# Kernel tuning notes

Measured on AMD Instinct MI355X. Metric: run time of the kernel, lower is better.

Reference implementation:

```python
import jax, jax.numpy as jnp
import numpy as np

B, T, N = 16, 1024, 128
WIN, STEP = 30, 2
MOMENT_ORDERS = (2, 4, 8)
D_MODEL = 256


def _mask_diag(corr):
    n = corr.shape[-1]
    eye = jnp.eye(n, dtype=corr.dtype)
    return corr * (1.0 - eye) + eye


def corrcoef_time(xw):
    # xw: [..., L, N] -> corr over channels: [..., N, N]
    L = xw.shape[-2]
    xm = xw - xw.mean(axis=-2, keepdims=True)
    cov = jnp.einsum('...ln,...lm->...nm', xm, xm) / (L - 1 + 1e-8)
    var = jnp.clip(jnp.diagonal(cov, axis1=-2, axis2=-1), 1e-8, None)
    std = jnp.sqrt(var)
    corr = cov / (std[..., :, None] * std[..., None, :])
    corr = jnp.nan_to_num(corr, nan=0.0, posinf=0.0, neginf=0.0)
    return _mask_diag(corr)


def rowwise_corr(M):
    # M: [B, N, F]
    Xc = M - M.mean(axis=-1, keepdims=True)
    num = jnp.einsum('bnf,bmf->bnm', Xc, Xc)
    den1 = jnp.sqrt(jnp.clip((Xc ** 2).sum(axis=-1), 1e-8, None))
    corr = num / (den1[:, :, None] * den1[:, None, :])
    corr = jnp.nan_to_num(corr, nan=0.0, posinf=0.0, neginf=0.0)
    return _mask_diag(corr)


def layer_norm(x, gamma, beta, eps=1e-5):
    mu = x.mean(axis=-1, keepdims=True)
    var = ((x - mu) ** 2).mean(axis=-1, keepdims=True)
    return (x - mu) / jnp.sqrt(var + eps) * gamma + beta


def normalize_adj(adj):
    n = adj.shape[-1]
    A_hat = adj + jnp.eye(n, dtype=adj.dtype)
    d = A_hat.sum(axis=-1)
    dis = jnp.sqrt(1.0 / jnp.clip(d, 1e-8, None))
    return A_hat * dis[:, :, None] * dis[:, None, :]


def setup_inputs() -> dict:
    key = jax.random.key(0)
    ks = jax.random.split(key, 8)
    in_dim = len(MOMENT_ORDERS) * N
    return {
        'x': jax.random.normal(ks[0], (B, T, N), dtype=jnp.float32),
        'ln_gamma': jnp.ones((in_dim,), jnp.float32),
        'ln_beta': jnp.zeros((in_dim,), jnp.float32),
        'W1': jax.random.normal(ks[1], (in_dim, D_MODEL), jnp.float32) * 0.05,
        'b1': jnp.zeros((D_MODEL,), jnp.float32),
        'W2': jax.random.normal(ks[2], (D_MODEL, D_MODEL), jnp.float32) * 0.05,
        'b2': jnp.zeros((D_MODEL,), jnp.float32),
        'Wc': jax.random.normal(ks[3], (D_MODEL, 1), jnp.float32) * 0.05,
        'bc': jnp.zeros((1,), jnp.float32),
    }


def reference(x, ln_gamma, ln_beta, W1, b1, W2, b2, Wc, bc):
    # sliding windows (static indices)
    starts = np.arange(0, T - WIN + 1, STEP)
    idx = starts[:, None] + np.arange(WIN)[None, :]
    xw = x[:, idx, :]
    lo = corrcoef_time(xw)                            # [B, Wn, N, N]

    mean_lo = lo.mean(axis=1, keepdims=True)
    centered = lo - mean_lo
    cm_list, ho_list = [], []
    for d in MOMENT_ORDERS:
        cm = jnp.nan_to_num((centered ** d).mean(axis=1),
                            nan=0.0, posinf=0.0, neginf=0.0)  # [B, N, N]
        cm_list.append(cm)
        ho_list.append(rowwise_corr(cm))

    X = jnp.concatenate(cm_list, axis=-1)             # [B, N, 3N]
    X = layer_norm(X, ln_gamma, ln_beta)

    A = jnp.stack(ho_list, axis=1).mean(axis=1)
    A = 0.5 * (A + jnp.swapaxes(A, 1, 2))
    A_norm = normalize_adj(A)

    H = jax.nn.relu(jnp.einsum('bnm,bmd->bnd', A_norm, X @ W1 + b1))
    H = jax.nn.relu(jnp.einsum('bnm,bmd->bnd', A_norm, H @ W2 + b2))
    g = H.mean(axis=1)                                # [B, d_model]
    out = jax.nn.sigmoid(g @ Wc + bc)                 # [B, 1]
    return out
```

## Files before the change

kernel.cpp:

```cpp
#include <hip/hip_runtime.h>
#include <math.h>

#define BB  16
#define TT  1024
#define NN  128
#define WIN 30
#define NWD 498
#define DM  256
#define IND 384
#define GW  16

#define INV_W (1.0f/498.0f)

#define SARR (BB*NN*NN)

#define OFF_A     0
#define OFF_G     (OFF_A    + BB*NWD*NN)
#define OFF_CM2   (OFF_G    + BB*NWD*NN)
#define OFF_CM4   (OFF_CM2  + SARR)
#define OFF_CM8   (OFF_CM4  + SARR)
#define OFF_AD    (OFF_CM8  + SARR)
#define OFF_PART  (OFF_AD   + 3*SARR)
#define OFF_ANORM OFF_PART
#define OFF_BUFA  (OFF_ANORM + SARR)
#define OFF_BUFB  (OFF_BUFA + BB*NN*DM)
#define OFF_CTR   (OFF_PART + 768*16384)

#define GLL16(gsrc, ldst) \
    __builtin_amdgcn_global_load_lds((const __attribute__((address_space(1))) void*)(gsrc), \
                                     (__attribute__((address_space(3))) void*)(ldst), 16, 0, 0)

__global__ __launch_bounds__(128) void k1_stats(const float* __restrict__ x, float* __restrict__ ws) {
    int bx = blockIdx.x;
    if (bx == 0 && threadIdx.x < 128) ((unsigned*)(ws + OFF_CTR))[threadIdx.x] = 0u;
    int c = bx & 15, b = bx >> 4;
    int w0 = c*32, w1 = min(NWD, w0+32);
    int n = threadIdx.x;
    const float* xp = x + (size_t)b*TT*NN + n;

    float sum = 0.f, sq = 0.f;
    for (int t = 2*w0; t < 2*w0 + WIN; ++t) {
        float v = xp[(size_t)t*NN];
        sum += v; sq = fmaf(v, v, sq);
    }
    for (int w = w0; w < w1; ++w) {
        if (w > w0) {
            float o0 = xp[(size_t)(2*w-2)*NN], o1 = xp[(size_t)(2*w-1)*NN];
            float n0 = xp[(size_t)(2*w+28)*NN], n1 = xp[(size_t)(2*w+29)*NN];
            sum += (n0 + n1) - (o0 + o1);
            sq  += (n0*n0 + n1*n1) - (o0*o0 + o1*o1);
        }
        float mean = sum * (1.0f/30.0f);
        float ss = sq - 30.0f*mean*mean;
        float var = fmaxf(ss * (1.0f/29.0f), 1e-8f);
        float a = (1.0f / sqrtf(var)) * 0.185695338f;
        ws[OFF_A + ((size_t)b*NWD + w)*NN + n] = a;
        ws[OFF_G + ((size_t)b*NWD + w)*NN + n] = mean * a * 5.477225575f;
    }
}

__global__ __launch_bounds__(256) __attribute__((amdgpu_waves_per_eu(3, 3)))
void k24_inc(const float* __restrict__ x, float* __restrict__ ws) {
    __shared__ __align__(16) float xr[64][NN];
    __shared__ __align__(16) float sa[GW][NN];
    __shared__ __align__(16) float sg[GW][NN];
    int bx = blockIdx.x;
    int wc = bx & 7;
    int slab = (bx >> 3) % 6;
    int b = bx / 48;
    const char IS[6] = {0,0,0,0,1,1};
    const char JS[6] = {0,1,2,3,2,3};
    int is = IS[slab], js = JS[slab];
    int w0 = wc * 63, w1 = min(NWD, w0 + 63);
    int tid = threadIdx.x;
    int jg = tid & 7, ig = tid >> 3;
    int i0 = is*64 + ig*2;
    int j0 = js*32 + jg*4;

    const float* xb = x + (size_t)b*TT*NN;
    const float* Ab = ws + OFF_A + (size_t)b*NWD*NN;
    const float* Gb = ws + OFF_G + (size_t)b*NWD*NN;

    float P[2][4];
    float S1[2][4], S2[2][4], S3[2][4], S4[2][4], S5[2][4], S6[2][4], S7[2][4], S8[2][4];
#pragma unroll
    for (int p=0;p<2;++p)
#pragma unroll
        for (int q=0;q<4;++q) {
            P[p][q]=0.f;
            S1[p][q]=0.f;S2[p][q]=0.f;S3[p][q]=0.f;S4[p][q]=0.f;
            S5[p][q]=0.f;S6[p][q]=0.f;S7[p][q]=0.f;S8[p][q]=0.f;
        }

    auto moments = [&](int k) {
        float2 ai = *(const float2*)&sa[k][i0];
        float2 gi = *(const float2*)&sg[k][i0];
        float4 aj = *(const float4*)&sa[k][j0];
        float4 gj = *(const float4*)&sg[k][j0];
        float av[2] = {ai.x, ai.y};
        float mg[2] = {-gi.x, -gi.y};
        float aw[4] = {aj.x, aj.y, aj.z, aj.w};
        float gw[4] = {gj.x, gj.y, gj.z, gj.w};
#pragma unroll
        for (int p=0;p<2;++p)
#pragma unroll
            for (int q=0;q<4;++q) {
                float aa  = av[p]*aw[q];
                float ngg = mg[p]*gw[q];
                float c   = fmaf(P[p][q], aa, ngg);
                float c2 = c*c;
                float c3 = c2*c;
                float c4 = c2*c2;
                S1[p][q] += c;
                S2[p][q] += c2;
                S3[p][q] += c3;
                S4[p][q] += c4;
                S5[p][q] = fmaf(c4, c,  S5[p][q]);
                S6[p][q] = fmaf(c3, c3, S6[p][q]);
                S7[p][q] = fmaf(c3, c4, S7[p][q]);
                S8[p][q] = fmaf(c4, c4, S8[p][q]);
            }
    };

    int rlo = 2*w0;
    for (int wg = w0; wg < w1; wg += GW) {
        int m = min(GW, w1 - wg);
        __syncthreads();
        int rhi = 2*(wg + m - 1) + 29;
        int nr = rhi - rlo + 1;
        for (int idx = tid; idx < nr*32; idx += 256) {
            int r = idx >> 5, c4 = idx & 31;
            int t = rlo + r;
            GLL16(xb + (size_t)t*NN + c4*4, &xr[t & 63][c4*4]);
        }
        for (int idx = tid; idx < m*32; idx += 256) {
            int k = idx >> 5, c4 = idx & 31;
            GLL16(Ab + (size_t)(wg+k)*NN + c4*4, &sa[k][c4*4]);
        }
        for (int idx = tid; idx < m*32; idx += 256) {
            int k = idx >> 5, c4 = idx & 31;
            GLL16(Gb + (size_t)(wg+k)*NN + c4*4, &sg[k][c4*4]);
        }
        rlo = rhi + 1;
        __syncthreads();

        int kstart = 0;
        if (wg == w0) {
#pragma unroll 6
            for (int k = 0; k < WIN; ++k) {
                int t = 2*w0 + k;
                float2 xi = *(const float2*)&xr[t & 63][i0];
                float4 xj = *(const float4*)&xr[t & 63][j0];
                float av[2] = {xi.x, xi.y};
                float bv[4] = {xj.x, xj.y, xj.z, xj.w};
#pragma unroll
                for (int p=0;p<2;++p)
#pragma unroll
                    for (int q=0;q<4;++q) P[p][q] = fmaf(av[p], bv[q], P[p][q]);
            }
            moments(0);
            kstart = 1;
        }
        for (int k = kstart; k < m; ++k) {
            int w = wg + k;
            int tr[4] = {2*w - 2, 2*w - 1, 2*w + 28, 2*w + 29};
#pragma unroll
            for (int kk = 0; kk < 4; ++kk) {
                int t = tr[kk];
                float sgn = (kk < 2) ? -1.0f : 1.0f;
                float2 xi = *(const float2*)&xr[t & 63][i0];
                float4 xj = *(const float4*)&xr[t & 63][j0];
                float av[2] = {sgn*xi.x, sgn*xi.y};
                float bv[4] = {xj.x, xj.y, xj.z, xj.w};
#pragma unroll
                for (int p=0;p<2;++p)
#pragma unroll
                    for (int q=0;q<4;++q) P[p][q] = fmaf(av[p], bv[q], P[p][q]);
            }
            moments(k);
        }
    }

    float* tp = ws + OFF_PART + (size_t)bx*16384 + tid*8;
#define STORE_ARR(A, S) \
    *(float4*)&tp[(A)*2048]     = make_float4(S[0][0], S[0][1], S[0][2], S[0][3]); \
    *(float4*)&tp[(A)*2048 + 4] = make_float4(S[1][0], S[1][1], S[1][2], S[1][3]);
    STORE_ARR(0, S1) STORE_ARR(1, S2) STORE_ARR(2, S3) STORE_ARR(3, S4)
    STORE_ARR(4, S5) STORE_ARR(5, S6) STORE_ARR(6, S7) STORE_ARR(7, S8)
#undef STORE_ARR
}

__global__ __launch_bounds__(256) void kred(float* __restrict__ ws) {
    int pair = blockIdx.x >> 3, sub = blockIdx.x & 7;
    int b = pair / 6, slab = pair % 6;
    const char IS[6] = {0,0,0,0,1,1};
    const char JS[6] = {0,1,2,3,2,3};
    int is = IS[slab], js = JS[slab];
    int off = sub*256 + threadIdx.x;
    const float* base = ws + OFF_PART + (size_t)(b*48 + slab*8)*16384;

    float E[8];
#pragma unroll
    for (int a=0;a<8;++a) E[a] = 0.f;
    for (int c = 0; c < 8; ++c) {
        const float* tp = base + (size_t)c*16384;
#pragma unroll
        for (int a=0;a<8;++a) E[a] += tp[a*2048 + off];
    }

    int tid_old = off >> 3, e = off & 7;
    int ig = tid_old >> 3, jg = tid_old & 7;
    int p = e >> 2, q = e & 3;
    int i = is*64 + ig*2 + p;
    int j = js*32 + jg*4 + q;

    float cm2, cm4, cm8;
    if (i == j) {
        cm2 = 0.f; cm4 = 0.f; cm8 = 0.f;
    } else {
        float e1 = E[0]*INV_W, e2 = E[1]*INV_W, e3 = E[2]*INV_W, e4 = E[3]*INV_W;
        float e5 = E[4]*INV_W, e6 = E[5]*INV_W, e7 = E[6]*INV_W, e8 = E[7]*INV_W;
        float m  = e1;
        float m2 = m*m, m3 = m2*m, m4 = m2*m2, m5 = m4*m, m6 = m3*m3, m8 = m4*m4;
        cm2 = e2 - m2;
        cm4 = e4 - 4.f*m*e3 + 6.f*m2*e2 - 3.f*m4;
        cm8 = e8 - 8.f*m*e7 + 28.f*m2*e6 - 56.f*m3*e5 + 70.f*m4*e4
                 - 56.f*m5*e3 + 28.f*m6*e2 - 7.f*m8;
    }
    float* C2 = ws + OFF_CM2 + (size_t)b*NN*NN;
    float* C4 = ws + OFF_CM4 + (size_t)b*NN*NN;
    float* C8 = ws + OFF_CM8 + (size_t)b*NN*NN;
    C2[i*NN + j] = cm2; C2[j*NN + i] = cm2;
    C4[i*NN + j] = cm4; C4[j*NN + i] = cm4;
    C8[i*NN + j] = cm8; C8[j*NN + i] = cm8;
}

#define XSTR 132
__global__ __launch_bounds__(256) void kB(const float* __restrict__ gamma, const float* __restrict__ beta,
                                          const float* __restrict__ W1, const float* __restrict__ b1,
                                          float* __restrict__ ws) {
    __shared__ __align__(16) float smem[64*XSTR + 2*NN];
    __shared__ unsigned winB;
    int blk = blockIdx.x, tid = threadIdx.x;
    if (blk < 192) {
        int rem = blk % 12;
        int b = blk / 12, di = rem >> 2, jq = rem & 3;
        float* Xct = smem;
        float* Mr  = smem + 64*XSTR;
        float* Ir  = Mr + NN;
        const float* cm = ws + (di==0 ? OFF_CM2 : (di==1 ? OFF_CM4 : OFF_CM8)) + (size_t)b*NN*NN;
        int n0 = (tid >> 4)*8, m0 = jq*32 + (tid & 15)*2;
        float s1 = 0.f, s2 = 0.f;
        float acc0[8], acc1[8];
#pragma unroll
        for (int k=0;k<8;++k) { acc0[k]=0.f; acc1[k]=0.f; }

        for (int h = 0; h < 2; ++h) {
            __syncthreads();
            for (int idx = tid; idx < NN*64; idx += 256) {
                int n = idx >> 6, f0 = idx & 63;
                Xct[f0*XSTR + n] = cm[n*NN + h*64 + f0];
            }
            __syncthreads();
            if (tid < NN) {
                for (int f0 = 0; f0 < 64; ++f0) {
                    float v = Xct[f0*XSTR + tid];
                    s1 += v; s2 = fmaf(v, v, s2);
                }
            }
            for (int f0 = 0; f0 < 64; ++f0) {
                const float* row = &Xct[f0*XSTR];
                float4 a0 = *(const float4*)&row[n0];
                float4 a1 = *(const float4*)&row[n0+4];
                float2 bm = *(const float2*)&row[m0];
                float av[8] = {a0.x,a0.y,a0.z,a0.w,a1.x,a1.y,a1.z,a1.w};
#pragma unroll
                for (int k=0;k<8;++k) {
                    acc0[k] = fmaf(av[k], bm.x, acc0[k]);
                    acc1[k] = fmaf(av[k], bm.y, acc1[k]);
                }
            }
        }
        __syncthreads();
        if (tid < NN) {
            float mean = s1 * (1.0f/NN);
            Mr[tid] = mean;
            Ir[tid] = 1.0f/sqrtf(fmaxf(s2 - (float)NN*mean*mean, 1e-8f));
        }
        __syncthreads();
        float rm0 = Mr[m0], rm1 = Mr[m0+1], im0 = Ir[m0], im1 = Ir[m0+1];
        float* Ad = ws + OFF_AD + (size_t)(b*3 + di)*NN*NN;
#pragma unroll
        for (int k=0;k<8;++k) {
            int gi = n0+k;
            float rn = Mr[gi], inv = Ir[gi];
            float v0 = (acc0[k] - (float)NN*rn*rm0) * inv * im0;
            float v1 = (acc1[k] - (float)NN*rn*rm1) * inv * im1;
            if (gi == m0)   v0 = 1.0f;
            if (gi == m0+1) v1 = 1.0f;
            Ad[gi*NN + m0]     = v0;
            Ad[gi*NN + m0 + 1] = v1;
        }

        __syncthreads();
        if (tid == 0) {
            unsigned* ctr = (unsigned*)(ws + OFF_CTR);
            unsigned old = __hip_atomic_fetch_add(&ctr[96 + b], 1u,
                                                  __ATOMIC_ACQ_REL, __HIP_MEMORY_SCOPE_AGENT);
            winB = (old == 11u) ? 1u : 0u;
        }
        __syncthreads();
        if (winB) {
            float* dis = smem;
            const float* A0 = ws + OFF_AD + (size_t)(b*3 + 0)*NN*NN;
            const float* A1 = ws + OFF_AD + (size_t)(b*3 + 1)*NN*NN;
            const float* A2 = ws + OFF_AD + (size_t)(b*3 + 2)*NN*NN;
            if (tid < NN) {
                float d = 1.0f;
                for (int m = 0; m < NN; ++m) {
                    int o = tid*NN + m;
                    d += (A0[o] + A1[o] + A2[o]) * (1.0f/3.0f);
                }
                dis[tid] = sqrtf(1.0f / fmaxf(d, 1e-8f));
            }
            __syncthreads();
            float* An = ws + OFF_ANORM + (size_t)b*NN*NN;
            for (int idx = tid; idx < NN*NN; idx += 256) {
                int n = idx >> 7, m = idx & 127;
                float s = (A0[idx] + A1[idx] + A2[idx]) * (1.0f/3.0f);
                float v = s + (n==m ? 1.0f : 0.0f);
                An[idx] = v * dis[n] * dis[m];
            }
        }
    } else {
        int r0 = (blk - 192) * 8;
        float* Xs = smem;
        float* sm = smem + 8*IND;
        float* sr = sm + 8;
        for (int r = 0; r < 8; ++r) {
            int row = r0 + r;
            int b = row >> 7, n = row & 127;
            const float* c2 = ws + OFF_CM2 + ((size_t)b*NN + n)*NN;
            const float* c4 = ws + OFF_CM4 + ((size_t)b*NN + n)*NN;
            const float* c8 = ws + OFF_CM8 + ((size_t)b*NN + n)*NN;
            for (int c = tid; c < IND; c += 256)
                Xs[r*IND+c] = (c < 128) ? c2[c] : (c < 256) ? c4[c-128] : c8[c-256];
        }
        __syncthreads();
        {
            int team = tid >> 5, lane = tid & 31;
            float s = 0.f;
            for (int c = lane; c < IND; c += 32) s += Xs[team*IND + c];
#pragma unroll
            for (int o = 16; o > 0; o >>= 1) s += __shfl_down(s, o, 32);
            float mean = __shfl(s, 0, 32) * (1.0f/IND);
            float v = 0.f;
            for (int c = lane; c < IND; c += 32) { float d = Xs[team*IND + c] - mean; v = fmaf(d, d, v); }
#pragma unroll
            for (int o = 16; o > 0; o >>= 1) v += __shfl_down(v, o, 32);
            if (lane == 0) {
                sm[team] = mean;
                sr[team] = 1.0f / sqrtf(v*(1.0f/IND) + 1e-5f);
            }
        }
        __syncthreads();
        for (int r = 0; r < 8; ++r) {
            float mean = sm[r], rstd = sr[r];
            for (int c = tid; c < IND; c += 256)
                Xs[r*IND+c] = (Xs[r*IND+c] - mean)*rstd*gamma[c] + beta[c];
        }
        __syncthreads();
        float acc[8];
        float bv = b1[tid];
#pragma unroll
        for (int r = 0; r < 8; ++r) acc[r] = bv;
        for (int kk = 0; kk < IND; kk += 4) {
            float w0 = W1[(size_t)(kk+0)*DM + tid];
            float w1 = W1[(size_t)(kk+1)*DM + tid];
            float w2 = W1[(size_t)(kk+2)*DM + tid];
            float w3 = W1[(size_t)(kk+3)*DM + tid];
#pragma unroll
            for (int r = 0; r < 8; ++r) {
                float4 xv = *(const float4*)&Xs[r*IND + kk];
                acc[r] = fmaf(xv.x, w0, acc[r]);
                acc[r] = fmaf(xv.y, w1, acc[r]);
                acc[r] = fmaf(xv.z, w2, acc[r]);
                acc[r] = fmaf(xv.w, w3, acc[r]);
            }
        }
        float* O = ws + OFF_BUFA;
#pragma unroll
        for (int r = 0; r < 8; ++r) O[(size_t)(r0+r)*DM + tid] = acc[r];
    }
}

__global__ __launch_bounds__(256) void k98_propgemm(const float* __restrict__ W2, const float* __restrict__ b2,
                                                    const float* __restrict__ An, const float* __restrict__ Zin,
                                                    float* __restrict__ Out) {
    __shared__ float Hs[8][DM];
    int bx = blockIdx.x;
    int b = bx >> 4, n0 = (bx & 15)*8;
    int tid = threadIdx.x;
    const float* A = An + (size_t)b*NN*NN + (size_t)n0*NN;
    const float* Z = Zin + (size_t)b*NN*DM;
    float acc[8] = {0,0,0,0,0,0,0,0};
    for (int m = 0; m < NN; m += 4) {
        float z0 = Z[(size_t)(m+0)*DM + tid];
        float z1 = Z[(size_t)(m+1)*DM + tid];
        float z2 = Z[(size_t)(m+2)*DM + tid];
        float z3 = Z[(size_t)(m+3)*DM + tid];
#pragma unroll
        for (int r = 0; r < 8; ++r) {
            const float* Ar = A + r*NN + m;
            acc[r] = fmaf(Ar[0], z0, acc[r]);
            acc[r] = fmaf(Ar[1], z1, acc[r]);
            acc[r] = fmaf(Ar[2], z2, acc[r]);
            acc[r] = fmaf(Ar[3], z3, acc[r]);
        }
    }
#pragma unroll
    for (int r = 0; r < 8; ++r) Hs[r][tid] = fmaxf(acc[r], 0.0f);
    __syncthreads();
    float acc2[8];
    float bv = b2[tid];
#pragma unroll
    for (int r = 0; r < 8; ++r) acc2[r] = bv;
    for (int k = 0; k < DM; k += 4) {
        float w0 = W2[(size_t)(k+0)*DM + tid];
        float w1 = W2[(size_t)(k+1)*DM + tid];
        float w2 = W2[(size_t)(k+2)*DM + tid];
        float w3 = W2[(size_t)(k+3)*DM + tid];
#pragma unroll
        for (int r = 0; r < 8; ++r) {
            float4 h = *(const float4*)&Hs[r][k];
            acc2[r] = fmaf(h.x, w0, acc2[r]);
            acc2[r] = fmaf(h.y, w1, acc2[r]);
            acc2[r] = fmaf(h.z, w2, acc2[r]);
            acc2[r] = fmaf(h.w, w3, acc2[r]);
        }
    }
    float* O = Out + (size_t)b*NN*DM;
#pragma unroll
    for (int r = 0; r < 8; ++r) O[(size_t)(n0+r)*DM + tid] = acc2[r];
}

__global__ __launch_bounds__(256) void k9_prop(const float* __restrict__ Wc, const float* __restrict__ bc,
                                               const float* __restrict__ An, const float* __restrict__ Zin,
                                               float* __restrict__ Out,
                                               float* __restrict__ ws, float* __restrict__ outp) {
    __shared__ float red[256];
    __shared__ unsigned win9;
    int bx = blockIdx.x;
    int b = bx >> 4, n0 = (bx & 15)*8;
    int tid = threadIdx.x;
    const float* A = An + (size_t)b*NN*NN + (size_t)n0*NN;
    const float* Z = Zin + (size_t)b*NN*DM;
    float acc[8] = {0,0,0,0,0,0,0,0};
    for (int m = 0; m < NN; m += 4) {
        float z0 = Z[(size_t)(m+0)*DM + tid];
        float z1 = Z[(size_t)(m+1)*DM + tid];
        float z2 = Z[(size_t)(m+2)*DM + tid];
        float z3 = Z[(size_t)(m+3)*DM + tid];
#pragma unroll
        for (int r = 0; r < 8; ++r) {
            const float* Ar = A + r*NN + m;
            acc[r] = fmaf(Ar[0], z0, acc[r]);
            acc[r] = fmaf(Ar[1], z1, acc[r]);
            acc[r] = fmaf(Ar[2], z2, acc[r]);
            acc[r] = fmaf(Ar[3], z3, acc[r]);
        }
    }
    float* O = Out + (size_t)b*NN*DM;
#pragma unroll
    for (int r = 0; r < 8; ++r) O[(size_t)(n0+r)*DM + tid] = fmaxf(acc[r], 0.0f);

    __syncthreads();
    if (tid == 0) {
        unsigned* ctr = (unsigned*)(ws + OFF_CTR);
        unsigned old = __hip_atomic_fetch_add(&ctr[112 + b], 1u,
                                              __ATOMIC_ACQ_REL, __HIP_MEMORY_SCOPE_AGENT);
        win9 = (old == 15u) ? 1u : 0u;
    }
    __syncthreads();
    if (win9) {
        const float* H = Out + (size_t)b*NN*DM;
        float s = 0.f;
        for (int n = 0; n < NN; ++n) s += H[(size_t)n*DM + tid];
        red[tid] = s * (1.0f/NN) * Wc[tid];
        __syncthreads();
        for (int o = 128; o > 0; o >>= 1) { if (tid < o) red[tid] += red[tid+o]; __syncthreads(); }
        if (tid == 0) outp[b] = 1.0f/(1.0f + expf(-(red[0] + bc[0])));
    }
}

extern "C" void kernel_launch(void* const* d_in, const int* in_sizes, int n_in,
                              void* d_out, int out_size, void* d_ws, size_t ws_size,
                              hipStream_t stream) {
    (void)in_sizes; (void)n_in; (void)out_size; (void)ws_size;
    const float* x     = (const float*)d_in[0];
    const float* gamma = (const float*)d_in[1];
    const float* beta  = (const float*)d_in[2];
    const float* W1    = (const float*)d_in[3];
    const float* b1    = (const float*)d_in[4];
    const float* W2    = (const float*)d_in[5];
    const float* b2    = (const float*)d_in[6];
    const float* Wc    = (const float*)d_in[7];
    const float* bc    = (const float*)d_in[8];
    float* ws  = (float*)d_ws;
    float* out = (float*)d_out;

    k1_stats    <<<BB*16,  128, 0, stream>>>(x, ws);
    k24_inc     <<<BB*6*8, 256, 0, stream>>>(x, ws);
    kred        <<<BB*6*8, 256, 0, stream>>>(ws);
    kB          <<<448,    256, 0, stream>>>(gamma, beta, W1, b1, ws);
    k98_propgemm<<<BB*16,  256, 0, stream>>>(W2, b2, ws + OFF_ANORM, ws + OFF_BUFA, ws + OFF_BUFB);
    k9_prop     <<<BB*16,  256, 0, stream>>>(Wc, bc, ws + OFF_ANORM, ws + OFF_BUFB, ws + OFF_BUFA, ws, out);
}
```

Measured before the change: 238.5 us.

## Fold LayerNorm affine into W1 and skip normalized X staging in kB

Precomputes gamma-scaled W1 and the column sums gamma·W1 and beta·W1 inside extra blocks of the reduction kernel. The LayerNorm+W1 GEMM can then run directly on the raw cm rows, applying mean and rstd afterwards as rstd*(acc - mean*sg) + sb. This removes the per-row LDS staging, the normalize pass and two barriers. Rows per block drop from 8 to 4, giving more blocks. Variance now comes from E[x²]-mean², which risks cancellation error, and W1 preprocessing is redone on every call.

```diff
diff --git a/kernel.cpp b/kernel.cpp
--- a/kernel.cpp
+++ b/kernel.cpp
@@ -25,6 +25,9 @@
 #define OFF_BUFA  (OFF_ANORM + SARR)
 #define OFF_BUFB  (OFF_BUFA + BB*NN*DM)
 #define OFF_CTR   (OFF_PART + 768*16384)
+#define OFF_GW1   OFF_A
+#define OFF_SG    (OFF_GW1 + IND*DM)
+#define OFF_SB    (OFF_SG  + DM)
 
 #define GLL16(gsrc, ldst) \
     __builtin_amdgcn_global_load_lds((const __attribute__((address_space(1))) void*)(gsrc), \
@@ -190,13 +193,36 @@
 #undef STORE_ARR
 }
 
-__global__ __launch_bounds__(256) void kred(float* __restrict__ ws) {
-    int pair = blockIdx.x >> 3, sub = blockIdx.x & 7;
+__global__ __launch_bounds__(256) void kred(const float* __restrict__ gamma, const float* __restrict__ beta,
+                                            const float* __restrict__ W1, float* __restrict__ ws) {
+    int bxg = blockIdx.x;
+    int tid = threadIdx.x;
+    if (bxg >= 768) {
+        int gi = bxg - 768;
+        if (gi < 96) {
+#pragma unroll
+            for (int kk = 0; kk < 4; ++kk) {
+                int k = gi*4 + kk;
+                ws[OFF_GW1 + (size_t)k*DM + tid] = gamma[k] * W1[(size_t)k*DM + tid];
+            }
+        } else {
+            float sgv = 0.f, sbv = 0.f;
+            for (int k = 0; k < IND; ++k) {
+                float w = W1[(size_t)k*DM + tid];
+                sgv = fmaf(gamma[k], w, sgv);
+                sbv = fmaf(beta[k],  w, sbv);
+            }
+            ws[OFF_SG + tid] = sgv;
+            ws[OFF_SB + tid] = sbv;
+        }
+        return;
+    }
+    int pair = bxg >> 3, sub = bxg & 7;
     int b = pair / 6, slab = pair % 6;
     const char IS[6] = {0,0,0,0,1,1};
     const char JS[6] = {0,1,2,3,2,3};
     int is = IS[slab], js = JS[slab];
-    int off = sub*256 + threadIdx.x;
+    int off = sub*256 + tid;
     const float* base = ws + OFF_PART + (size_t)(b*48 + slab*8)*16384;
 
     float E[8];
@@ -236,9 +262,7 @@
 }
 
 #define XSTR 132
-__global__ __launch_bounds__(256) void kB(const float* __restrict__ gamma, const float* __restrict__ beta,
-                                          const float* __restrict__ W1, const float* __restrict__ b1,
-                                          float* __restrict__ ws) {
+__global__ __launch_bounds__(256) void kB(const float* __restrict__ b1, float* __restrict__ ws) {
     __shared__ __align__(16) float smem[64*XSTR + 2*NN];
     __shared__ unsigned winB;
     int blk = blockIdx.x, tid = threadIdx.x;
@@ -333,64 +357,66 @@
             }
         }
     } else {
-        int r0 = (blk - 192) * 8;
-        float* Xs = smem;
-        float* sm = smem + 8*IND;
-        float* sr = sm + 8;
-        for (int r = 0; r < 8; ++r) {
-            int row = r0 + r;
-            int b = row >> 7, n = row & 127;
+        int r0 = (blk - 192) * 4;
+        float* sms = smem;
+        float* srs = smem + 4;
+        {
+            int rloc = tid >> 6, lane = tid & 63;
+            int grow = r0 + rloc;
+            int b = grow >> 7, n = grow & 127;
             const float* c2 = ws + OFF_CM2 + ((size_t)b*NN + n)*NN;
             const float* c4 = ws + OFF_CM4 + ((size_t)b*NN + n)*NN;
             const float* c8 = ws + OFF_CM8 + ((size_t)b*NN + n)*NN;
-            for (int c = tid; c < IND; c += 256)
-                Xs[r*IND+c] = (c < 128) ? c2[c] : (c < 256) ? c4[c-128] : c8[c-256];
-        }
-        __syncthreads();
-        {
-            int team = tid >> 5, lane = tid & 31;
-            float s = 0.f;
-            for (int c = lane; c < IND; c += 32) s += Xs[team*IND + c];
-#pragma unroll
-            for (int o = 16; o > 0; o >>= 1) s += __shfl_down(s, o, 32);
-            float mean = __shfl(s, 0, 32) * (1.0f/IND);
-            float v = 0.f;
-            for (int c = lane; c < IND; c += 32) { float d = Xs[team*IND + c] - mean; v = fmaf(d, d, v); }
-#pragma unroll
-            for (int o = 16; o > 0; o >>= 1) v += __shfl_down(v, o, 32);
+            float s1 = 0.f, s2 = 0.f;
+            for (int e = lane; e < IND; e += 64) {
+                float v = (e < 128) ? c2[e] : (e < 256) ? c4[e-128] : c8[e-256];
+                s1 += v; s2 = fmaf(v, v, s2);
+            }
+#pragma unroll
+            for (int o = 32; o > 0; o >>= 1) {
+                s1 += __shfl_down(s1, o, 64);
+                s2 += __shfl_down(s2, o, 64);
+            }
             if (lane == 0) {
-                sm[team] = mean;
-                sr[team] = 1.0f / sqrtf(v*(1.0f/IND) + 1e-5f);
-            }
-        }
-        __syncthreads();
-        for (int r = 0; r < 8; ++r) {
-            float mean = sm[r], rstd = sr[r];
-            for (int c = tid; c < IND; c += 256)
-                Xs[r*IND+c] = (Xs[r*IND+c] - mean)*rstd*gamma[c] + beta[c];
-        }
-        __syncthreads();
-        float acc[8];
-        float bv = b1[tid];
-#pragma unroll
-        for (int r = 0; r < 8; ++r) acc[r] = bv;
-        for (int kk = 0; kk < IND; kk += 4) {
-            float w0 = W1[(size_t)(kk+0)*DM + tid];
-            float w1 = W1[(size_t)(kk+1)*DM + tid];
-            float w2 = W1[(size_t)(kk+2)*DM + tid];
-            float w3 = W1[(size_t)(kk+3)*DM + tid];
-#pragma unroll
-            for (int r = 0; r < 8; ++r) {
-                float4 xv = *(const float4*)&Xs[r*IND + kk];
-                acc[r] = fmaf(xv.x, w0, acc[r]);
-                acc[r] = fmaf(xv.y, w1, acc[r]);
-                acc[r] = fmaf(xv.z, w2, acc[r]);
-                acc[r] = fmaf(xv.w, w3, acc[r]);
-            }
-        }
+                float mean = s1 * (1.0f/IND);
+                sms[rloc] = mean;
+                srs[rloc] = 1.0f / sqrtf(s2*(1.0f/IND) - mean*mean + 1e-5f);
+            }
+        }
+        __syncthreads();
+        float mean[4], rstd[4];
+        const float* xrow[4];
+#pragma unroll
+        for (int r = 0; r < 4; ++r) {
+            mean[r] = sms[r]; rstd[r] = srs[r];
+        }
+        float acc[4] = {0.f, 0.f, 0.f, 0.f};
+        const float* GW1p = ws + OFF_GW1;
+#pragma unroll
+        for (int seg = 0; seg < 3; ++seg) {
+            int offc = (seg==0) ? OFF_CM2 : (seg==1) ? OFF_CM4 : OFF_CM8;
+#pragma unroll
+            for (int r = 0; r < 4; ++r) {
+                int grow = r0 + r;
+                xrow[r] = ws + offc + ((size_t)(grow >> 7)*NN + (grow & 127))*NN;
+            }
+            const float* gseg = GW1p + (size_t)(seg*128)*DM + tid;
+            for (int k = 0; k < 128; k += 2) {
+                float g0 = gseg[(size_t)(k+0)*DM];
+                float g1 = gseg[(size_t)(k+1)*DM];
+#pragma unroll
+                for (int r = 0; r < 4; ++r) {
+                    acc[r] = fmaf(xrow[r][k+0], g0, acc[r]);
+                    acc[r] = fmaf(xrow[r][k+1], g1, acc[r]);
+                }
+            }
+        }
+        float sgv = ws[OFF_SG + tid];
+        float sbb = ws[OFF_SB + tid] + b1[tid];
         float* O = ws + OFF_BUFA;
 #pragma unroll
-        for (int r = 0; r < 8; ++r) O[(size_t)(r0+r)*DM + tid] = acc[r];
+        for (int r = 0; r < 4; ++r)
+            O[(size_t)(r0+r)*DM + tid] = rstd[r]*(acc[r] - mean[r]*sgv) + sbb;
     }
 }
 
@@ -509,10 +535,10 @@
     float* ws  = (float*)d_ws;
     float* out = (float*)d_out;
 
-    k1_stats    <<<BB*16,  128, 0, stream>>>(x, ws);
-    k24_inc     <<<BB*6*8, 256, 0, stream>>>(x, ws);
-    kred        <<<BB*6*8, 256, 0, stream>>>(ws);
-    kB          <<<448,    256, 0, stream>>>(gamma, beta, W1, b1, ws);
-    k98_propgemm<<<BB*16,  256, 0, stream>>>(W2, b2, ws + OFF_ANORM, ws + OFF_BUFA, ws + OFF_BUFB);
-    k9_prop     <<<BB*16,  256, 0, stream>>>(Wc, bc, ws + OFF_ANORM, ws + OFF_BUFB, ws + OFF_BUFA, ws, out);
-}
+    k1_stats    <<<BB*16,    128, 0, stream>>>(x, ws);
+    k24_inc     <<<BB*6*8,   256, 0, stream>>>(x, ws);
+    kred        <<<768+96+1, 256, 0, stream>>>(gamma, beta, W1, ws);
+    kB          <<<704,      256, 0, stream>>>(b1, ws);
+    k98_propgemm<<<BB*16,    256, 0, stream>>>(W2, b2, ws + OFF_ANORM, ws + OFF_BUFA, ws + OFF_BUFB);
+    k9_prop     <<<BB*16,    256, 0, stream>>>(Wc, bc, ws + OFF_ANORM, ws + OFF_BUFB, ws + OFF_BUFA, ws, out);
+}
```

After: 233.5 us. -2.1%, faster.
